# Kernel optimization log

Hardware: AMD Instinct MI355X
Metric: run time of the kernel (lower is better)

Reference implementation:

```python
import jax, jax.numpy as jnp
import numpy as np
from jax import lax

SD = 16          # sample_duration
STRIDE = 16      # feat_stride
SCALES = (4, 8, 16)
RATIOS = (0.5, 1.0, 2.0)
PRE_NMS = 1000   # proposals kept before NMS (TEST config)
POST_NMS = 128   # proposals kept after NMS
NMS_TH = 0.7


def _anchors2d():
    base = 16.0
    ctr = (base - 1.0) / 2.0
    out = []
    for r in RATIOS:
        ws = np.round(np.sqrt(base * base / r))
        hs = np.round(ws * r)
        for s in SCALES:
            w, h = ws * s, hs * s
            out.append([ctr - (w - 1) / 2, ctr - (h - 1) / 2,
                        ctr + (w - 1) / 2, ctr + (h - 1) / 2])
    return np.asarray(out, np.float32)                       # (9, 4)


def _anchors3d():
    # tube anchors: (x1, y1, t1, x2, y2, t2), durations [SD, SD/2, SD/4]
    a2 = _anchors2d()
    out = []
    for d in (SD, SD // 2, SD // 4):
        for a in a2:
            out.append([a[0], a[1], 0.0, a[2], a[3], d - 1.0])
    return np.asarray(out, np.float32)                       # (27, 6)


def _shifted(anchors, H, W):
    k = anchors.shape[-1]
    sx = jnp.arange(W, dtype=jnp.float32) * STRIDE
    sy = jnp.arange(H, dtype=jnp.float32) * STRIDE
    if k == 4:
        sh = jnp.stack(jnp.broadcast_arrays(sx[None, :], sy[:, None],
                                            sx[None, :], sy[:, None]), -1)
    else:
        z = jnp.zeros((H, W), jnp.float32)
        sh = jnp.stack(jnp.broadcast_arrays(sx[None, :], sy[:, None], z,
                                            sx[None, :], sy[:, None], z), -1)
    return (sh[:, :, None, :] + jnp.asarray(anchors)[None, None]).reshape(-1, k)


def _decode(anchors, deltas):
    # deltas layout: (d_ctr..., d_logsize...); works for 2D (k=4) and 3D (k=6)
    nd = anchors.shape[-1] // 2
    lo, hi = anchors[..., :nd], anchors[..., nd:]
    size = hi - lo + 1.0
    ctr = lo + 0.5 * (size - 1.0)
    pctr = deltas[..., :nd] * size + ctr
    psize = jnp.exp(deltas[..., nd:]) * size
    return jnp.concatenate([pctr - 0.5 * (psize - 1.0),
                            pctr + 0.5 * (psize - 1.0)], -1)


def _iou(b, boxes):
    # b: (k,), boxes: (N, k); area/volume IoU with +1 pixel convention
    nd = boxes.shape[-1] // 2
    lo = jnp.maximum(b[:nd], boxes[:, :nd])
    hi = jnp.minimum(b[nd:], boxes[:, nd:])
    inter = jnp.prod(jnp.maximum(hi - lo + 1.0, 0.0), -1)
    va = jnp.prod(b[nd:] - b[:nd] + 1.0)
    vb = jnp.prod(boxes[:, nd:] - boxes[:, :nd] + 1.0, -1)
    return inter / (va + vb - inter)


def _nms(boxes):
    # boxes already sorted by descending score; greedy NMS, fixed output size
    N = boxes.shape[0]

    def body(i, c):
        supp, keep = c
        idx = jnp.argmax(~supp)                 # first unsuppressed box
        keep = keep.at[i].set(idx.astype(jnp.int32))
        supp = supp | (_iou(boxes[idx], boxes) > NMS_TH)
        supp = supp.at[idx].set(True)
        return supp, keep

    _, keep = lax.fori_loop(0, POST_NMS, body,
                            (jnp.zeros(N, bool), jnp.zeros(POST_NMS, jnp.int32)))
    return keep


def _proposals(scores, deltas, anchors, maxs):
    # scores (B,N), deltas (B,N,k), anchors (N,k), maxs (B,1,k)
    boxes = jnp.clip(_decode(anchors[None], deltas), 0.0, maxs)
    _, idx = lax.top_k(scores, PRE_NMS)
    bx = jnp.take_along_axis(boxes, idx[..., None], axis=1)   # (B,PRE,k)
    keep = jax.vmap(_nms)(bx)                                 # (B,POST)
    sel = jnp.take_along_axis(bx, keep[..., None], axis=1)    # (B,POST,k)
    bidx = jnp.broadcast_to(
        jnp.arange(sel.shape[0], dtype=sel.dtype)[:, None, None],
        sel.shape[:2] + (1,))
    return lax.stop_gradient(jnp.concatenate([bidx, sel], -1))


def setup_inputs() -> dict:
    k = jax.random.split(jax.random.key(0), 8)
    s = 0.01
    return {
        "base_feat": jax.random.normal(k[0], (1, 256, 16, 32, 32), jnp.float32),
        "im_info": jnp.array([[512.0, 512.0, 1.0]], jnp.float32),
        "gt_boxes": jax.random.uniform(k[1], (1, 5, 7), jnp.float32) * 100.0,
        "gt_rois": jax.random.uniform(k[2], (1, 5, 16, 5), jnp.float32) * 100.0,
        "W_conv": jax.random.normal(k[3], (512, 256, 3, 3, 3), jnp.float32) * s,
        "b_conv": jnp.zeros((512,), jnp.float32),
        "W_cls": jax.random.normal(k[4], (54, 512), jnp.float32) * s,
        "b_cls": jnp.zeros((54,), jnp.float32),
        "W_bbox": jax.random.normal(k[5], (162, 512), jnp.float32) * s,
        "b_bbox": jnp.zeros((162,), jnp.float32),
        "W_cls16": jax.random.normal(k[6], (18, 512), jnp.float32) * s,
        "b_cls16": jnp.zeros((18,), jnp.float32),
        "W_bbox16": jax.random.normal(k[7], (36, 512), jnp.float32) * s,
        "b_bbox16": jnp.zeros((36,), jnp.float32),
    }


def reference(base_feat, im_info, gt_boxes, gt_rois, W_conv, b_conv,
              W_cls, b_cls, W_bbox, b_bbox, W_cls16, b_cls16,
              W_bbox16, b_bbox16):
    B, _, T, H, W = base_feat.shape
    # RPN_Conv: 3x3x3 Conv3d + ReLU
    conv1 = jax.nn.relu(
        lax.conv_general_dilated(base_feat, W_conv, (1, 1, 1), "SAME",
                                 dimension_numbers=("NCDHW", "OIDHW", "NCDHW"))
        + b_conv[None, :, None, None, None])
    # 1x1x1 score / bbox heads (3D)
    cls3 = jnp.einsum("bcthw,oc->bothw", conv1, W_cls) + b_cls[None, :, None, None, None]
    bbox3 = jnp.einsum("bcthw,oc->bothw", conv1, W_bbox) + b_bbox[None, :, None, None, None]
    # permute(0,1,3,4,2).mean(4) == mean over the temporal axis
    feat2 = conv1.mean(axis=2)
    cls2 = jnp.einsum("bchw,oc->bohw", feat2, W_cls16) + b_cls16[None, :, None, None]
    bbox2 = jnp.einsum("bchw,oc->bohw", feat2, W_bbox16) + b_bbox16[None, :, None, None]
    # reshape(x,2) + softmax over dim 1; fg prob is the second half of channels
    fg3 = jax.nn.softmax(cls3.reshape(B, 2, 27, T, H, W), axis=1)[:, 1]  # (B,27,T,H,W)
    fg2 = jax.nn.softmax(cls2.reshape(B, 2, 9, H, W), axis=1)[:, 1]      # (B,9,H,W)
    # proposal layers consume detached tensors (torch .data)
    fg3, fg2, bbox3d, bbox2d = map(lax.stop_gradient, (fg3, fg2, bbox3, bbox2))
    # flatten position-major (h, w, anchor)
    sc3 = fg3.mean(axis=2).transpose(0, 2, 3, 1).reshape(B, -1)
    dl3 = bbox3d.mean(axis=2).reshape(B, 27, 6, H, W).transpose(0, 3, 4, 1, 2).reshape(B, -1, 6)
    sc2 = fg2.transpose(0, 2, 3, 1).reshape(B, -1)
    dl2 = bbox2d.reshape(B, 9, 4, H, W).transpose(0, 3, 4, 1, 2).reshape(B, -1, 4)
    imh, imw = im_info[:, 0][:, None], im_info[:, 1][:, None]
    sdm = jnp.full_like(imw, SD - 1.0)
    max3 = jnp.stack([imw - 1, imh - 1, sdm, imw - 1, imh - 1, sdm], -1)  # (B,1,6)
    max2 = jnp.stack([imw - 1, imh - 1, imw - 1, imh - 1], -1)            # (B,1,4)
    rois = _proposals(sc3, dl3, _shifted(_anchors3d(), H, W), max3)       # (B,POST,7)
    rois16 = _proposals(sc2, dl2, _shifted(_anchors2d(), H, W), max2)     # (B,POST,5)
    z = jnp.zeros((), jnp.float32)  # eval mode: all RPN losses are 0
    return rois, rois16, z, z, z, z
```

## Files before the change

### kernel.cpp

```cpp
#include <hip/hip_runtime.h>
#include <hip/hip_bf16.h>
#include <cfloat>
#include <cstdint>


#define T_DIM 16
#define H_DIM 32
#define W_DIM 32
#define NVOX  (T_DIM*H_DIM*W_DIM)
#define HW    (H_DIM*W_DIM)
#define CIN   256
#define COUT  512
#define PRE_NMS 1000
#define POST_NMS 128
#define NMS_TH 0.7f

typedef __attribute__((ext_vector_type(8))) short v8s;
typedef __attribute__((ext_vector_type(4))) float v4f;
typedef __attribute__((ext_vector_type(4))) int v4i;

#define MFMA_B16(A,B,C) __builtin_amdgcn_mfma_f32_16x16x32_bf16(A,B,C,0,0,0)

__device__ __forceinline__ short f2bf(float x) {
    unsigned u = __float_as_uint(x);
    u += 0x7FFFu + ((u >> 16) & 1u);
    return (short)(u >> 16);
}
__device__ __forceinline__ float bf2f(short s) {
    return __uint_as_float(((unsigned)(unsigned short)s) << 16);
}
__device__ __forceinline__ int pk(short a, short b) {
    return (int)((unsigned short)a | ((unsigned)(unsigned short)b << 16));
}

__constant__ float c_ws[3] = {23.f, 16.f, 11.f};
__constant__ float c_hs[3] = {12.f, 16.f, 22.f};
__constant__ float c_sc[3] = {4.f, 8.f, 16.f};
__constant__ float c_depth[3] = {16.f, 8.f, 4.f};

__global__ void k_split_w(const float* __restrict__ W, short* __restrict__ A0,
                          short* __restrict__ A1, short* __restrict__ A2) {
    int i = blockIdx.x * 256 + threadIdx.x;
    int c = i & 255;
    int o = (i >> 8) & 511;
    int tap = i >> 17;
    float x = W[(o * 256 + c) * 27 + tap];
    short h = f2bf(x); float r = x - bf2f(h);
    short m = f2bf(r); float r2 = r - bf2f(m);
    short l = f2bf(r2);
    A0[i] = h; A1[i] = m; A2[i] = l;
}

__global__ void k_build_wcomb(const float* __restrict__ Wcls, const float* __restrict__ Wbb,
                              float* __restrict__ Wc) {
    int i = blockIdx.x * 256 + threadIdx.x;
    int o = i & 255;
    int c = i >> 8;
    float v = 0.f;
    if (o < 54) v = Wcls[o * 512 + c];
    else if (o < 216) v = Wbb[(o - 54) * 512 + c];
    Wc[i] = v;
}

#define SP8(X0,X1,X2,X3,X4,X5,X6,X7, OH, OM, OL) {                            \
    short h0_=f2bf(X0), h1_=f2bf(X1), h2_=f2bf(X2), h3_=f2bf(X3);             \
    short h4_=f2bf(X4), h5_=f2bf(X5), h6_=f2bf(X6), h7_=f2bf(X7);             \
    float r0_=(X0)-bf2f(h0_), r1_=(X1)-bf2f(h1_), r2_=(X2)-bf2f(h2_);         \
    float r3_=(X3)-bf2f(h3_), r4_=(X4)-bf2f(h4_), r5_=(X5)-bf2f(h5_);         \
    float r6_=(X6)-bf2f(h6_), r7_=(X7)-bf2f(h7_);                             \
    short m0_=f2bf(r0_), m1_=f2bf(r1_), m2_=f2bf(r2_), m3_=f2bf(r3_);         \
    short m4_=f2bf(r4_), m5_=f2bf(r5_), m6_=f2bf(r6_), m7_=f2bf(r7_);         \
    short l0_=f2bf(r0_-bf2f(m0_)), l1_=f2bf(r1_-bf2f(m1_));                   \
    short l2_=f2bf(r2_-bf2f(m2_)), l3_=f2bf(r3_-bf2f(m3_));                   \
    short l4_=f2bf(r4_-bf2f(m4_)), l5_=f2bf(r5_-bf2f(m5_));                   \
    short l6_=f2bf(r6_-bf2f(m6_)), l7_=f2bf(r7_-bf2f(m7_));                   \
    OH = (v4i){pk(h0_,h1_), pk(h2_,h3_), pk(h4_,h5_), pk(h6_,h7_)};           \
    OM = (v4i){pk(m0_,m1_), pk(m2_,m3_), pk(m4_,m5_), pk(m6_,m7_)};           \
    OL = (v4i){pk(l0_,l1_), pk(l2_,l3_), pk(l4_,l5_), pk(l6_,l7_)};           \
}

#define CV_SHIFT(TAP) {                                                       \
    int kt_ = (TAP) / 9 - 1, kh_ = ((TAP) / 3) % 3 - 1, kw_ = (TAP) % 3 - 1;  \
    int tt_ = bt + kt_, hh_ = bh + kh_, ww_ = bw + kw_;                       \
    bVal = ((unsigned)tt_ < 16u) && ((unsigned)hh_ < 32u) && ((unsigned)ww_ < 32u); \
    bOff = bVal ? ((tt_ << 10) + (hh_ << 5) + ww_) : 0;                       \
}

#define CV_LOAD_A(TAP, CK) {                                                  \
    size_t ao_ = ((size_t)((TAP) * 512 + o0 + sr) << 8) + (CK) + skh * 16;    \
    pa0 = *(const v4i*)(A0 + ao_); pa1 = *(const v4i*)(A0 + ao_ + 8);         \
    pa2 = *(const v4i*)(A1 + ao_); pa3 = *(const v4i*)(A1 + ao_ + 8);         \
    pa4 = *(const v4i*)(A2 + ao_); pa5 = *(const v4i*)(A2 + ao_ + 8);         \
}

#define CV_LOAD_B(CK) {                                                       \
    const float* ip_ = I + ((size_t)((CK) + skh * 16) << 14) + bOff;          \
    float x0_  = bVal ? ip_[0]        : 0.f;                                  \
    float x1_  = bVal ? ip_[1 << 14]  : 0.f;                                  \
    float x2_  = bVal ? ip_[2 << 14]  : 0.f;                                  \
    float x3_  = bVal ? ip_[3 << 14]  : 0.f;                                  \
    float x4_  = bVal ? ip_[4 << 14]  : 0.f;                                  \
    float x5_  = bVal ? ip_[5 << 14]  : 0.f;                                  \
    float x6_  = bVal ? ip_[6 << 14]  : 0.f;                                  \
    float x7_  = bVal ? ip_[7 << 14]  : 0.f;                                  \
    float x8_  = bVal ? ip_[8 << 14]  : 0.f;                                  \
    float x9_  = bVal ? ip_[9 << 14]  : 0.f;                                  \
    float x10_ = bVal ? ip_[10 << 14] : 0.f;                                  \
    float x11_ = bVal ? ip_[11 << 14] : 0.f;                                  \
    float x12_ = bVal ? ip_[12 << 14] : 0.f;                                  \
    float x13_ = bVal ? ip_[13 << 14] : 0.f;                                  \
    float x14_ = bVal ? ip_[14 << 14] : 0.f;                                  \
    float x15_ = bVal ? ip_[15 << 14] : 0.f;                                  \
    SP8(x0_,x1_,x2_,x3_,x4_,x5_,x6_,x7_,       pbh0, pbm0, pbl0);             \
    SP8(x8_,x9_,x10_,x11_,x12_,x13_,x14_,x15_, pbh1, pbm1, pbl1);             \
}

__global__ __launch_bounds__(256) void k_conv3d_mfma(
        const float* __restrict__ I, const short* __restrict__ A0,
        const short* __restrict__ A1, const short* __restrict__ A2,
        const float* __restrict__ bias, float* __restrict__ O) {
    __shared__ v4i Ash[3][512];
    __shared__ v4i Bsh[3][512];
    const int tid = threadIdx.x;
    const int o0 = blockIdx.y * 128;
    const int v0 = blockIdx.x * 128;
    const int lane = tid & 63;
    const int wv = tid >> 6;
    const int quad = lane >> 4, m16 = lane & 15;
    const int wo = (wv >> 1) * 64;
    const int wvx = (wv & 1) * 64;

    const int sr = ((tid >> 6) & 1) * 64 + (tid & 63);
    const int skh = tid >> 7;
    const int uW0 = sr * 4 + ((skh * 2) ^ ((sr >> 2) & 3));
    const int uW1 = sr * 4 + ((skh * 2 + 1) ^ ((sr >> 2) & 3));

    const int vbase = v0 + sr;
    const int bt = vbase >> 10, bh = (vbase >> 5) & 31, bw = vbase & 31;

    const int sw = quad ^ (m16 >> 2);
    const int uA = (wo + m16) * 4 + sw;
    const int uB = (wvx + m16) * 4 + sw;

    v4f acc[4][4];
#pragma unroll
    for (int i = 0; i < 4; i++)
#pragma unroll
        for (int j = 0; j < 4; j++) acc[i][j] = (v4f){0.f, 0.f, 0.f, 0.f};

    int bOff, bVal;
    v4i pa0, pa1, pa2, pa3, pa4, pa5;
    v4i pbh0, pbh1, pbm0, pbm1, pbl0, pbl1;

    CV_SHIFT(0);
    CV_LOAD_A(0, 0);
    CV_LOAD_B(0);

    for (int s = 0; s < 216; ++s) {
        __syncthreads();
        Ash[0][uW0] = pa0; Ash[0][uW1] = pa1;
        Ash[1][uW0] = pa2; Ash[1][uW1] = pa3;
        Ash[2][uW0] = pa4; Ash[2][uW1] = pa5;
        Bsh[0][uW0] = pbh0; Bsh[0][uW1] = pbh1;
        Bsh[1][uW0] = pbm0; Bsh[1][uW1] = pbm1;
        Bsh[2][uW0] = pbl0; Bsh[2][uW1] = pbl1;
        __syncthreads();
        {
            int s1 = s + 1;
            if (s1 < 216) {
                int tap1 = s1 >> 3, ck1 = (s1 & 7) << 5;
                if ((s1 & 7) == 0) CV_SHIFT(tap1);
                CV_LOAD_A(tap1, ck1);
                CV_LOAD_B(ck1);
            }
        }
        v8s ah0 = *(const v8s*)(&Ash[0][uA]);
        v8s ah1 = *(const v8s*)(&Ash[0][uA + 64]);
        v8s ah2 = *(const v8s*)(&Ash[0][uA + 128]);
        v8s ah3 = *(const v8s*)(&Ash[0][uA + 192]);
        v8s am0 = *(const v8s*)(&Ash[1][uA]);
        v8s am1 = *(const v8s*)(&Ash[1][uA + 64]);
        v8s am2 = *(const v8s*)(&Ash[1][uA + 128]);
        v8s am3 = *(const v8s*)(&Ash[1][uA + 192]);
        v8s al0 = *(const v8s*)(&Ash[2][uA]);
        v8s al1 = *(const v8s*)(&Ash[2][uA + 64]);
        v8s al2 = *(const v8s*)(&Ash[2][uA + 128]);
        v8s al3 = *(const v8s*)(&Ash[2][uA + 192]);
#pragma unroll
        for (int j = 0; j < 4; ++j) {
            v8s bb = *(const v8s*)(&Bsh[0][uB + j * 64]);
            v8s bm = *(const v8s*)(&Bsh[1][uB + j * 64]);
            v8s bl = *(const v8s*)(&Bsh[2][uB + j * 64]);
            v4f a;
            a = acc[0][j];
            a = MFMA_B16(ah0, bb, a); a = MFMA_B16(ah0, bm, a);
            a = MFMA_B16(am0, bb, a); a = MFMA_B16(ah0, bl, a);
            a = MFMA_B16(am0, bm, a); a = MFMA_B16(al0, bb, a);
            acc[0][j] = a;
            a = acc[1][j];
            a = MFMA_B16(ah1, bb, a); a = MFMA_B16(ah1, bm, a);
            a = MFMA_B16(am1, bb, a); a = MFMA_B16(ah1, bl, a);
            a = MFMA_B16(am1, bm, a); a = MFMA_B16(al1, bb, a);
            acc[1][j] = a;
            a = acc[2][j];
            a = MFMA_B16(ah2, bb, a); a = MFMA_B16(ah2, bm, a);
            a = MFMA_B16(am2, bb, a); a = MFMA_B16(ah2, bl, a);
            a = MFMA_B16(am2, bm, a); a = MFMA_B16(al2, bb, a);
            acc[2][j] = a;
            a = acc[3][j];
            a = MFMA_B16(ah3, bb, a); a = MFMA_B16(ah3, bm, a);
            a = MFMA_B16(am3, bb, a); a = MFMA_B16(ah3, bl, a);
            a = MFMA_B16(am3, bm, a); a = MFMA_B16(al3, bb, a);
            acc[3][j] = a;
        }
    }

#pragma unroll
    for (int i = 0; i < 4; ++i) {
#pragma unroll
        for (int r = 0; r < 4; ++r) {
            int o = o0 + wo + i * 16 + quad * 4 + r;
            float bo = bias[o];
            float* dst = O + (size_t)o * NVOX + v0 + wvx + m16;
#pragma unroll
            for (int j = 0; j < 4; ++j)
                dst[j * 16] = fmaxf(acc[i][j][r] + bo, 0.f);
        }
    }
}

__global__ __launch_bounds__(256) void k_gemm_logits3(const float* __restrict__ conv1,
                                                      const float* __restrict__ Wc,
                                                      float* __restrict__ L) {
    __shared__ float As[16][128];
    __shared__ float Bs[16][128];
    const int tid = threadIdx.x;
    const int o0 = blockIdx.y * 128;
    const int v0 = blockIdx.x * 128;
    const int ty = tid >> 4, tx = tid & 15;

    float acc[8][8];
#pragma unroll
    for (int i = 0; i < 8; i++)
#pragma unroll
        for (int j = 0; j < 8; j++) acc[i][j] = 0.f;

    for (int ck = 0; ck < 512; ck += 16) {
        __syncthreads();
#pragma unroll
        for (int r = 0; r < 2; ++r) {
            int f = tid + r * 256;
            int c_l = f >> 5, o4 = (f & 31) << 2;
            *(float4*)(&As[c_l][o4]) = *(const float4*)(Wc + ((size_t)(ck + c_l) << 8) + o0 + o4);
        }
#pragma unroll
        for (int r = 0; r < 2; ++r) {
            int f = tid + r * 256;
            int c_l = f >> 5, v4 = (f & 31) << 2;
            *(float4*)(&Bs[c_l][v4]) = *(const float4*)(conv1 + ((size_t)(ck + c_l) << 14) + v0 + v4);
        }
        __syncthreads();
#pragma unroll
        for (int k = 0; k < 16; ++k) {
            float a[8], b[8];
            *(float4*)(a)     = *(const float4*)(&As[k][ty * 4]);
            *(float4*)(a + 4) = *(const float4*)(&As[k][64 + ty * 4]);
            *(float4*)(b)     = *(const float4*)(&Bs[k][tx * 4]);
            *(float4*)(b + 4) = *(const float4*)(&Bs[k][64 + tx * 4]);
#pragma unroll
            for (int i = 0; i < 8; i++)
#pragma unroll
                for (int j = 0; j < 8; j++)
                    acc[i][j] = fmaf(a[i], b[j], acc[i][j]);
        }
    }
#pragma unroll
    for (int i = 0; i < 8; i++) {
        int orow = (i < 4) ? (ty * 4 + i) : (64 + ty * 4 + (i - 4));
        float* dst = L + (size_t)(o0 + orow) * NVOX + v0;
        *(float4*)(dst + tx * 4)      = *(const float4*)(&acc[i][0]);
        *(float4*)(dst + 64 + tx * 4) = *(const float4*)(&acc[i][4]);
    }
}

__global__ void k_sc3(const float* __restrict__ L, const float* __restrict__ b_cls,
                      float* __restrict__ sc3) {
    int i = blockIdx.x * 256 + threadIdx.x;
    if (i >= 27 * HW) return;
    int a = i >> 10, hw = i & 1023;
    float b0 = b_cls[a], b1 = b_cls[27 + a];
    const float* L0 = L + (size_t)a * NVOX + hw;
    const float* L1 = L + (size_t)(27 + a) * NVOX + hw;
    float s = 0.f;
    for (int t = 0; t < T_DIM; t++) {
        float x0 = L0[t * HW] + b0, x1 = L1[t * HW] + b1;
        float m = fmaxf(x0, x1);
        float e0 = expf(x0 - m), e1 = expf(x1 - m);
        s += e1 / (e0 + e1);
    }
    sc3[hw * 27 + a] = s * (1.f / 16.f);
}

__global__ void k_dl3(const float* __restrict__ L, const float* __restrict__ b_bbox,
                      float* __restrict__ dl3) {
    int i = blockIdx.x * 256 + threadIdx.x;
    if (i >= 162 * HW) return;
    int ch = i >> 10, hw = i & 1023;
    const float* Lr = L + (size_t)(54 + ch) * NVOX + hw;
    float s = 0.f;
    for (int t = 0; t < T_DIM; t++) s += Lr[t * HW];
    s = s * (1.f / 16.f) + b_bbox[ch];
    int a = ch / 6, d = ch - a * 6;
    dl3[((size_t)hw * 27 + a) * 6 + d] = s;
}

__global__ void k_feat2(const float* __restrict__ conv1, float* __restrict__ feat2) {
    int i = blockIdx.x * 256 + threadIdx.x;
    int c = i >> 10, hw = i & 1023;
    const float* src = conv1 + (size_t)c * NVOX + hw;
    float s = 0.f;
    for (int t = 0; t < T_DIM; t++) s += src[t * HW];
    feat2[i] = s * (1.f / 16.f);
}

__global__ void k_gemm2d(const float* __restrict__ feat2, const float* __restrict__ Wcls16,
                         const float* __restrict__ Wbb16, float* __restrict__ L2) {
    int g = blockIdx.x * 256 + threadIdx.x;
    int o = g >> 10, hw = g & 1023;
    const float* wrow = (o < 18) ? (Wcls16 + (size_t)o * 512) : (Wbb16 + (size_t)(o - 18) * 512);
    float s = 0.f;
    for (int c = 0; c < 512; c++) s = fmaf(wrow[c], feat2[(size_t)c * HW + hw], s);
    L2[(size_t)o * HW + hw] = s;
}

__global__ void k_sc2(const float* __restrict__ L2, const float* __restrict__ b_cls16,
                      float* __restrict__ sc2) {
    int i = blockIdx.x * 256 + threadIdx.x;
    if (i >= 9 * HW) return;
    int a = i >> 10, hw = i & 1023;
    float x0 = L2[(size_t)a * HW + hw] + b_cls16[a];
    float x1 = L2[(size_t)(9 + a) * HW + hw] + b_cls16[9 + a];
    float m = fmaxf(x0, x1);
    float e0 = expf(x0 - m), e1 = expf(x1 - m);
    sc2[hw * 9 + a] = e1 / (e0 + e1);
}

__global__ void k_dl2(const float* __restrict__ L2, const float* __restrict__ b_bbox16,
                      float* __restrict__ dl2) {
    int i = blockIdx.x * 256 + threadIdx.x;
    if (i >= 36 * HW) return;
    int ch = i >> 10, hw = i & 1023;
    float v = L2[(size_t)(18 + ch) * HW + hw] + b_bbox16[ch];
    int a = ch >> 2, d = ch & 3;
    dl2[((size_t)hw * 9 + a) * 4 + d] = v;
}

__device__ __forceinline__ unsigned mapf(float f) {
    unsigned u = __float_as_uint(f);
    return (u & 0x80000000u) ? ~u : (u | 0x80000000u);
}

__global__ __launch_bounds__(1024) void k_proposal(const float* __restrict__ im_info,
                                                   const float* __restrict__ sc3,
                                                   const float* __restrict__ dl3,
                                                   const float* __restrict__ sc2,
                                                   const float* __restrict__ dl2,
                                                   float* __restrict__ out) {
    const int branch = blockIdx.x;
    const int tid = threadIdx.x;
    const int A = (branch == 0) ? 27 : 9;
    const int nd = (branch == 0) ? 3 : 2;
    const float* scores = (branch == 0) ? sc3 : sc2;
    const float* deltas = (branch == 0) ? dl3 : dl2;
    const int K = PRE_NMS;
    const int ept = A;
    const int base = tid * ept;

    __shared__ unsigned hist[256];
    __shared__ unsigned long long keys[1024];
    __shared__ float bx[PRE_NMS][6];
    __shared__ int keep[POST_NMS];
    __shared__ unsigned wsum[16];
    __shared__ unsigned long long alive[16];
    __shared__ int sh_b, sh_next, bcast;

    unsigned prefix = 0;
    int rank = K;
    for (int shift = 24; shift >= 0; shift -= 8) {
        if (tid < 256) hist[tid] = 0;
        __syncthreads();
        const unsigned mask_hi = (shift == 24) ? 0u : (0xFFFFFFFFu << (shift + 8));
        for (int j = 0; j < ept; j++) {
            unsigned m = mapf(scores[base + j]);
            if ((m & mask_hi) == prefix)
                atomicAdd(&hist[(m >> shift) & 255], 1u);
        }
        __syncthreads();
        for (int d = 1; d < 256; d <<= 1) {
            unsigned add = 0;
            if (tid < 256 && tid + d < 256) add = hist[tid + d];
            __syncthreads();
            if (tid < 256) hist[tid] += add;
            __syncthreads();
        }
        if (tid < 256) {
            bool win = (hist[tid] >= (unsigned)rank) &&
                       (tid == 255 || hist[tid + 1] < (unsigned)rank);
            if (win) { sh_b = tid; sh_next = (tid == 255) ? 0 : (int)hist[tid + 1]; }
        }
        __syncthreads();
        prefix |= (unsigned)sh_b << shift;
        rank -= sh_next;
        __syncthreads();
    }
    const unsigned tau = prefix;

    int gt_c = 0, eq_c = 0;
    for (int j = 0; j < ept; j++) {
        unsigned m = mapf(scores[base + j]);
        gt_c += (m > tau);
        eq_c += (m == tau);
    }
    unsigned cnt = ((unsigned)gt_c << 16) | (unsigned)eq_c;
    const int lane = tid & 63, wid = tid >> 6;
    unsigned x = cnt;
    for (int d = 1; d < 64; d <<= 1) {
        unsigned y = __shfl_up(x, d);
        if (lane >= d) x += y;
    }
    if (lane == 63) wsum[wid] = x;
    __syncthreads();
    if (wid == 0) {
        unsigned w = (lane < 16) ? wsum[lane] : 0;
        for (int d = 1; d < 16; d <<= 1) {
            unsigned y = __shfl_up(w, d);
            if (lane >= d) w += y;
        }
        if (lane < 16) wsum[lane] = w;
    }
    __syncthreads();
    unsigned excl = x - cnt + (wid ? wsum[wid - 1] : 0);
    const int c1 = (int)(wsum[15] >> 16);
    int gi = (int)(excl >> 16);
    int ei = (int)(excl & 0xFFFFu);
    for (int j = 0; j < ept; j++) {
        int idx = base + j;
        unsigned m = mapf(scores[idx]);
        unsigned long long key = ((unsigned long long)m << 32) |
                                 (unsigned)(0xFFFFFFFFu - (unsigned)idx);
        if (m > tau) {
            keys[gi++] = key;
        } else if (m == tau) {
            if (c1 + ei < K) keys[c1 + ei] = key;
            ei++;
        }
    }
    if (tid < 1024 - K) keys[K + tid] = 0;
    __syncthreads();

    for (int k = 2; k <= 1024; k <<= 1) {
        for (int j = k >> 1; j > 0; j >>= 1) {
            int ixj = tid ^ j;
            if (ixj > tid) {
                unsigned long long a = keys[tid], b = keys[ixj];
                bool sw2 = ((tid & k) == 0) ? (a < b) : (a > b);
                if (sw2) { keys[tid] = b; keys[ixj] = a; }
            }
            __syncthreads();
        }
    }

    const float imh = im_info[0], imw = im_info[1];
    if (tid < K) {
        int n = (int)(0xFFFFFFFFu - (unsigned)(keys[tid] & 0xFFFFFFFFull));
        int cell = n / A, a = n - cell * A;
        int hc = cell >> 5, wc = cell & 31;
        int a2 = (branch == 0) ? (a % 9) : a;
        int ri = a2 / 3, si = a2 % 3;
        float w = c_ws[ri] * c_sc[si], h = c_hs[ri] * c_sc[si];
        float lo[3], hi[3], mx[3];
        lo[0] = 7.5f - (w - 1.f) * 0.5f + 16.f * wc;
        hi[0] = 7.5f + (w - 1.f) * 0.5f + 16.f * wc;
        mx[0] = imw - 1.f;
        lo[1] = 7.5f - (h - 1.f) * 0.5f + 16.f * hc;
        hi[1] = 7.5f + (h - 1.f) * 0.5f + 16.f * hc;
        mx[1] = imh - 1.f;
        if (branch == 0) { lo[2] = 0.f; hi[2] = c_depth[a / 9] - 1.f; mx[2] = (float)(T_DIM - 1); }
        const float* dp = deltas + (size_t)n * (2 * nd);
        for (int d = 0; d < nd; d++) {
            float size = hi[d] - lo[d] + 1.f;
            float ctr = lo[d] + 0.5f * (size - 1.f);
            float pctr = dp[d] * size + ctr;
            float psize = expf(dp[nd + d]) * size;
            float pl = pctr - 0.5f * (psize - 1.f);
            float ph = pctr + 0.5f * (psize - 1.f);
            bx[tid][d]      = fminf(fmaxf(pl, 0.f), mx[d]);
            bx[tid][nd + d] = fminf(fmaxf(ph, 0.f), mx[d]);
        }
    }
    if (tid < 16) alive[tid] = (tid < 15) ? ~0ull : ((1ull << (K - 15 * 64)) - 1);
    __syncthreads();

    float myb[6]; float myvol = 1.f;
    if (tid < K) {
        for (int d = 0; d < 6; d++) myb[d] = bx[tid][d];
        for (int d = 0; d < nd; d++) myvol *= (myb[nd + d] - myb[d] + 1.f);
    }
    for (int i = 0; i < POST_NMS; ++i) {
        if (tid < 64) {
            unsigned long long wvb = (tid < 16) ? alive[tid] : 0ull;
            int cand = wvb ? (tid * 64 + __ffsll(wvb) - 1) : 0x7fffffff;
#pragma unroll
            for (int off = 32; off; off >>= 1)
                cand = min(cand, __shfl_xor(cand, off));
            if (tid == 0) {
                int m = (cand == 0x7fffffff) ? 0 : cand;
                bcast = m; keep[i] = m;
            }
        }
        __syncthreads();
        int sel = bcast;
        bool s = false;
        if (tid < K) {
            float inter = 1.f, selvol = 1.f;
            for (int d = 0; d < nd; d++) {
                float slo = bx[sel][d], shi = bx[sel][nd + d];
                float l = fmaxf(slo, myb[d]);
                float hh = fminf(shi, myb[nd + d]);
                inter *= fmaxf(hh - l + 1.f, 0.f);
                selvol *= (shi - slo + 1.f);
            }
            float iou = inter / (selvol + myvol - inter);
            s = (iou > NMS_TH) || (tid == sel);
        }
        unsigned long long bal = __ballot(s);
        if (lane == 0 && bal) alive[wid] &= ~bal;
        __syncthreads();
    }

    if (tid < POST_NMS) {
        int k = keep[tid];
        if (branch == 0) {
            float* o = out + (size_t)tid * 7;
            o[0] = 0.f;
            for (int d = 0; d < 6; d++) o[1 + d] = bx[k][d];
        } else {
            float* o = out + 128 * 7 + (size_t)tid * 5;
            o[0] = 0.f;
            for (int d = 0; d < 4; d++) o[1 + d] = bx[k][d];
        }
    }
    if (branch == 0 && tid == 0) {
        out[1536] = 0.f; out[1537] = 0.f; out[1538] = 0.f; out[1539] = 0.f;
    }
}

extern "C" void kernel_launch(void* const* d_in, const int* in_sizes, int n_in,
                              void* d_out, int out_size, void* d_ws, size_t ws_size,
                              hipStream_t stream) {
    (void)in_sizes; (void)n_in; (void)out_size; (void)ws_size;
    const float* base_feat = (const float*)d_in[0];
    const float* im_info   = (const float*)d_in[1];
    const float* W_conv    = (const float*)d_in[4];
    const float* b_conv    = (const float*)d_in[5];
    const float* W_cls     = (const float*)d_in[6];
    const float* b_cls     = (const float*)d_in[7];
    const float* W_bbox    = (const float*)d_in[8];
    const float* b_bbox    = (const float*)d_in[9];
    const float* W_cls16   = (const float*)d_in[10];
    const float* b_cls16   = (const float*)d_in[11];
    const float* W_bbox16  = (const float*)d_in[12];
    const float* b_bbox16  = (const float*)d_in[13];
    float* out = (float*)d_out;

    char* ws = (char*)d_ws;
    const size_t AW = (size_t)27 * 512 * 256;
    short* A0 = (short*)ws;
    short* A1 = A0 + AW;
    short* A2 = A1 + AW;
    float* L3 = (float*)ws;
    size_t off = AW * 3 * sizeof(short);
    float* Wcomb  = (float*)(ws + off); off += (size_t)512 * 256 * 4;
    float* conv1  = (float*)(ws + off); off += (size_t)COUT * NVOX * 4;
    float* feat2  = (float*)(ws + off); off += (size_t)512 * HW * 4;
    float* L2     = (float*)(ws + off); off += (size_t)64 * HW * 4;
    float* sc3    = (float*)(ws + off); off += (size_t)27 * HW * 4;
    float* dl3    = (float*)(ws + off); off += (size_t)27 * HW * 6 * 4;
    float* sc2    = (float*)(ws + off); off += (size_t)9 * HW * 4;
    float* dl2    = (float*)(ws + off); off += (size_t)9 * HW * 4 * 4;

    k_split_w<<<13824, 256, 0, stream>>>(W_conv, A0, A1, A2);
    k_build_wcomb<<<512, 256, 0, stream>>>(W_cls, W_bbox, Wcomb);
    {
        dim3 g(NVOX / 128, COUT / 128);
        k_conv3d_mfma<<<g, 256, 0, stream>>>(base_feat, A0, A1, A2, b_conv, conv1);
    }
    {
        dim3 g(NVOX / 128, 2);
        k_gemm_logits3<<<g, 256, 0, stream>>>(conv1, Wcomb, L3);
    }
    k_sc3<<<(27 * HW + 255) / 256, 256, 0, stream>>>(L3, b_cls, sc3);
    k_dl3<<<(162 * HW + 255) / 256, 256, 0, stream>>>(L3, b_bbox, dl3);
    k_feat2<<<(512 * HW) / 256, 256, 0, stream>>>(conv1, feat2);
    k_gemm2d<<<(54 * HW) / 256, 256, 0, stream>>>(feat2, W_cls16, W_bbox16, L2);
    k_sc2<<<(9 * HW + 255) / 256, 256, 0, stream>>>(L2, b_cls16, sc2);
    k_dl2<<<(36 * HW + 255) / 256, 256, 0, stream>>>(L2, b_bbox16, dl2);
    k_proposal<<<2, 1024, 0, stream>>>(im_info, sc3, dl3, sc2, dl2, out);
}
```

Measured before the change: 1.143 ms.

## Load conv weight fragments directly from global in MFMA layout, drop A LDS staging

Reorders the split bf16 weight buffers so each 8-element k-chunk is contiguous per output channel, letting each lane load its MFMA A operand straight from global memory instead of staging it through shared memory. It removes the Ash LDS array and its stores and reads, and changes the B shared layout and thread-to-row mapping to match. The cost is that A fragments are now fetched per wave, with redundant global/L2 traffic across waves and no prefetch one step ahead, so load latency sits directly before the MFMAs.

```diff
diff --git a/kernel.cpp b/kernel.cpp
--- a/kernel.cpp
+++ b/kernel.cpp
@@ -41,9 +41,11 @@
 __global__ void k_split_w(const float* __restrict__ W, short* __restrict__ A0,
                           short* __restrict__ A1, short* __restrict__ A2) {
     int i = blockIdx.x * 256 + threadIdx.x;
-    int c = i & 255;
-    int o = (i >> 8) & 511;
+    int c7 = i & 7;
+    int o = (i >> 3) & 511;
+    int ko = (i >> 12) & 31;
     int tap = i >> 17;
+    int c = ko * 8 + c7;
     float x = W[(o * 256 + c) * 27 + tap];
     short h = f2bf(x); float r = x - bf2f(h);
     short m = f2bf(r); float r2 = r - bf2f(m);
@@ -84,13 +86,6 @@
     int tt_ = bt + kt_, hh_ = bh + kh_, ww_ = bw + kw_;                       \
     bVal = ((unsigned)tt_ < 16u) && ((unsigned)hh_ < 32u) && ((unsigned)ww_ < 32u); \
     bOff = bVal ? ((tt_ << 10) + (hh_ << 5) + ww_) : 0;                       \
-}
-
-#define CV_LOAD_A(TAP, CK) {                                                  \
-    size_t ao_ = ((size_t)((TAP) * 512 + o0 + sr) << 8) + (CK) + skh * 16;    \
-    pa0 = *(const v4i*)(A0 + ao_); pa1 = *(const v4i*)(A0 + ao_ + 8);         \
-    pa2 = *(const v4i*)(A1 + ao_); pa3 = *(const v4i*)(A1 + ao_ + 8);         \
-    pa4 = *(const v4i*)(A2 + ao_); pa5 = *(const v4i*)(A2 + ao_ + 8);         \
 }
 
 #define CV_LOAD_B(CK) {                                                       \
@@ -119,7 +114,6 @@
         const float* __restrict__ I, const short* __restrict__ A0,
         const short* __restrict__ A1, const short* __restrict__ A2,
         const float* __restrict__ bias, float* __restrict__ O) {
-    __shared__ v4i Ash[3][512];
     __shared__ v4i Bsh[3][512];
     const int tid = threadIdx.x;
     const int o0 = blockIdx.y * 128;
@@ -130,17 +124,16 @@
     const int wo = (wv >> 1) * 64;
     const int wvx = (wv & 1) * 64;
 
-    const int sr = ((tid >> 6) & 1) * 64 + (tid & 63);
-    const int skh = tid >> 7;
-    const int uW0 = sr * 4 + ((skh * 2) ^ ((sr >> 2) & 3));
-    const int uW1 = sr * 4 + ((skh * 2 + 1) ^ ((sr >> 2) & 3));
-
-    const int vbase = v0 + sr;
+    const int sa_o = tid >> 1, skh = tid & 1;
+    const int uW0 = (skh * 2) * 128 + sa_o;
+    const int uW1 = (skh * 2 + 1) * 128 + sa_o;
+
+    const int vbase = v0 + sa_o;
     const int bt = vbase >> 10, bh = (vbase >> 5) & 31, bw = vbase & 31;
 
-    const int sw = quad ^ (m16 >> 2);
-    const int uA = (wo + m16) * 4 + sw;
-    const int uB = (wvx + m16) * 4 + sw;
+    const int uB = quad * 128 + wvx + m16;
+
+    const size_t aLane = ((size_t)(o0 + wo + m16) << 3) + ((size_t)quad << 12);
 
     v4f acc[4][4];
 #pragma unroll
@@ -149,48 +142,44 @@
         for (int j = 0; j < 4; j++) acc[i][j] = (v4f){0.f, 0.f, 0.f, 0.f};
 
     int bOff, bVal;
-    v4i pa0, pa1, pa2, pa3, pa4, pa5;
     v4i pbh0, pbh1, pbm0, pbm1, pbl0, pbl1;
 
     CV_SHIFT(0);
-    CV_LOAD_A(0, 0);
     CV_LOAD_B(0);
 
     for (int s = 0; s < 216; ++s) {
         __syncthreads();
-        Ash[0][uW0] = pa0; Ash[0][uW1] = pa1;
-        Ash[1][uW0] = pa2; Ash[1][uW1] = pa3;
-        Ash[2][uW0] = pa4; Ash[2][uW1] = pa5;
         Bsh[0][uW0] = pbh0; Bsh[0][uW1] = pbh1;
         Bsh[1][uW0] = pbm0; Bsh[1][uW1] = pbm1;
         Bsh[2][uW0] = pbl0; Bsh[2][uW1] = pbl1;
         __syncthreads();
+        const int tap = s >> 3;
+        const size_t aBase = (((size_t)tap * 32 + ((s & 7) << 2)) << 12) + aLane;
+        v8s ah0 = *(const v8s*)(A0 + aBase);
+        v8s ah1 = *(const v8s*)(A0 + aBase + 16 * 8);
+        v8s ah2 = *(const v8s*)(A0 + aBase + 32 * 8);
+        v8s ah3 = *(const v8s*)(A0 + aBase + 48 * 8);
+        v8s am0 = *(const v8s*)(A1 + aBase);
+        v8s am1 = *(const v8s*)(A1 + aBase + 16 * 8);
+        v8s am2 = *(const v8s*)(A1 + aBase + 32 * 8);
+        v8s am3 = *(const v8s*)(A1 + aBase + 48 * 8);
+        v8s al0 = *(const v8s*)(A2 + aBase);
+        v8s al1 = *(const v8s*)(A2 + aBase + 16 * 8);
+        v8s al2 = *(const v8s*)(A2 + aBase + 32 * 8);
+        v8s al3 = *(const v8s*)(A2 + aBase + 48 * 8);
         {
             int s1 = s + 1;
             if (s1 < 216) {
                 int tap1 = s1 >> 3, ck1 = (s1 & 7) << 5;
                 if ((s1 & 7) == 0) CV_SHIFT(tap1);
-                CV_LOAD_A(tap1, ck1);
                 CV_LOAD_B(ck1);
             }
         }
-        v8s ah0 = *(const v8s*)(&Ash[0][uA]);
-        v8s ah1 = *(const v8s*)(&Ash[0][uA + 64]);
-        v8s ah2 = *(const v8s*)(&Ash[0][uA + 128]);
-        v8s ah3 = *(const v8s*)(&Ash[0][uA + 192]);
-        v8s am0 = *(const v8s*)(&Ash[1][uA]);
-        v8s am1 = *(const v8s*)(&Ash[1][uA + 64]);
-        v8s am2 = *(const v8s*)(&Ash[1][uA + 128]);
-        v8s am3 = *(const v8s*)(&Ash[1][uA + 192]);
-        v8s al0 = *(const v8s*)(&Ash[2][uA]);
-        v8s al1 = *(const v8s*)(&Ash[2][uA + 64]);
-        v8s al2 = *(const v8s*)(&Ash[2][uA + 128]);
-        v8s al3 = *(const v8s*)(&Ash[2][uA + 192]);
 #pragma unroll
         for (int j = 0; j < 4; ++j) {
-            v8s bb = *(const v8s*)(&Bsh[0][uB + j * 64]);
-            v8s bm = *(const v8s*)(&Bsh[1][uB + j * 64]);
-            v8s bl = *(const v8s*)(&Bsh[2][uB + j * 64]);
+            v8s bb = *(const v8s*)(&Bsh[0][uB + j * 16]);
+            v8s bm = *(const v8s*)(&Bsh[1][uB + j * 16]);
+            v8s bl = *(const v8s*)(&Bsh[2][uB + j * 16]);
             v4f a;
             a = acc[0][j];
             a = MFMA_B16(ah0, bb, a); a = MFMA_B16(ah0, bm, a);
```

After: 983.3 us. -14.0%, faster.
